# Kernel optimization log

Measured on AMD Instinct MI355X. Metric: run time of the kernel, lower is better.

The kernel has to match this reference:

```python
import jax, jax.numpy as jnp
import numpy as np

N = 4096
REG_STRENGTH = 1.0
BLOCK_EPS = 1e-6  # tolerance for detecting pooled-block boundaries in the backward


@jax.custom_vjp
def isotonic_l2(y):
    """argmin_{v_1 >= v_2 >= ... >= v_n} 0.5 * ||v - y||^2 (PAV solution).

    Computed via the exact minimax characterization, fully vectorized:
        v_i = min_{j <= i} max_{k >= i} mean(y[j..k])
    """
    return _iso_solution(y)


def _iso_solution(y):
    n = y.shape[0]
    cs = jnp.concatenate([jnp.zeros((1,), y.dtype), jnp.cumsum(y)])  # [n+1]
    idx = jnp.arange(n)
    j = idx[:, None]  # block start
    k = idx[None, :]  # block end
    length = (k - j + 1).astype(y.dtype)
    A = (cs[k + 1] - cs[j]) / length            # mean(y[j..k]) where k >= j
    A = jnp.where(k >= j, A, -jnp.inf)
    # M[j, i] = max_{k >= i} A[j, k]  (reverse cumulative max along k)
    M = jnp.flip(jax.lax.cummax(jnp.flip(A, axis=1), axis=1), axis=1)
    # v_i = min_{j <= i} M[j, i]  (cumulative min along j, take diagonal)
    v = jnp.diagonal(jax.lax.cummin(M, axis=0))
    return v


def _iso_fwd(y):
    v = _iso_solution(y)
    return v, v


def _iso_bwd(v, g):
    # Jacobian of PAV: within each pooled block, grad is the block mean of g.
    n = v.shape[0]
    drop = (v[:-1] - v[1:]) > BLOCK_EPS * jnp.maximum(jnp.abs(v[:-1]), 1.0)
    bid = jnp.concatenate([jnp.zeros((1,), jnp.int32),
                           jnp.cumsum(drop.astype(jnp.int32))])
    sums = jax.ops.segment_sum(g, bid, num_segments=n)
    cnts = jax.ops.segment_sum(jnp.ones_like(g), bid, num_segments=n)
    return ((sums / jnp.maximum(cnts, 1.0))[bid],)


isotonic_l2.defvjp(_iso_fwd, _iso_bwd)


def soft_rank(x, regularization_strength):
    """torchsort-style L2 soft rank: project x/eps onto permutahedron P([n..1])."""
    n = x.shape[0]
    theta = x / regularization_strength
    perm = jnp.argsort(-theta)          # descending sort permutation (constant wrt grad)
    s = theta[perm]
    w = jnp.arange(n, 0, -1, dtype=x.dtype)  # [n, n-1, ..., 1]
    sol = isotonic_l2(s - w)
    ranks_sorted = s - sol
    inv = jnp.argsort(perm)
    return ranks_sorted[inv]


def setup_inputs() -> dict:
    key = jax.random.key(0)
    kp, kt = jax.random.split(key)
    pred = jax.random.normal(kp, (N,), dtype=jnp.float32)
    target = jax.random.normal(kt, (N,), dtype=jnp.float32)
    return {"pred": pred, "target": target}


def reference(pred, target):
    p = soft_rank(pred, REG_STRENGTH)
    t = soft_rank(target, REG_STRENGTH)
    p = p - p.mean()
    p = p / jnp.linalg.norm(p)
    t = t - t.mean()
    t = t / jnp.linalg.norm(t)
    return 1.0 - jnp.sum(p * t)
```

## Files before the change

kernel.cpp:

```cpp
#include <hip/hip_runtime.h>
#include <math.h>

#define NEL   4096
#define NT    1024
#define HALF  512
#define EPT   (NEL / HALF)
#define CB    256

__global__ __launch_bounds__(CB)
void count_kernel(const float* __restrict__ pred,
                  const float* __restrict__ target,
                  int* __restrict__ counts) {
  __shared__ float jv[CB];
  const int arr = blockIdx.z;
  const float* __restrict__ x = arr ? target : pred;
  const int i     = blockIdx.x * CB + threadIdx.x;
  const int jbase = blockIdx.y * CB;

  jv[threadIdx.x] = x[jbase + threadIdx.x];
  const float xi = x[i];
  __syncthreads();

  int c = 0;
#pragma unroll 8
  for (int t = 0; t < CB; t++) {
    const float v = jv[t];
    const int   j = jbase + t;
    c += (v > xi || (v == xi && j < i)) ? 1 : 0;
  }
  atomicAdd(&counts[arr * NEL + i], c);
}

__global__ __launch_bounds__(NT)
void pav_loss_kernel(const float* __restrict__ pred,
                     const float* __restrict__ target,
                     const int* __restrict__ counts,
                     float* __restrict__ loss_out) {
  __shared__ float  s_val[2][NEL];
  __shared__ double s_P[2][NEL + 1];
  __shared__ int    s_cnt[2][NEL];
  __shared__ double s_wsum[2][HALF / 64];
  __shared__ int    s_nb[2];
  __shared__ double s_red[NT / 64][5];

  const int tid  = threadIdx.x;
  const int arr  = tid >> 9;
  const int tA   = tid & (HALF - 1);
  const int lane = tid & 63;
  const int wA   = tA >> 6;
  const float* __restrict__ x = arr ? target : pred;
  const int* __restrict__ cnt = counts + arr * NEL;
  const int base = tA * EPT;

  int   r[EPT];
  float xv[EPT];
#pragma unroll
  for (int e = 0; e < EPT; e++) {
    const int i = base + e;
    xv[e] = x[i];
    r[e]  = cnt[i];
    s_val[arr][r[e]] = xv[e];
  }
  __syncthreads();

  double c[EPT];
  double acc = 0.0;
#pragma unroll
  for (int e = 0; e < EPT; e++) {
    const int p = base + e;
    acc += (double)s_val[arr][p] - (double)(NEL - p);
    c[e] = acc;
  }
  double sc = acc;
#pragma unroll
  for (int d = 1; d < 64; d <<= 1) {
    const double o = __shfl_up(sc, d, 64);
    if (lane >= d) sc += o;
  }
  if (lane == 63) s_wsum[arr][wA] = sc;
  __syncthreads();
  if (tA == 0) {
    double a2 = 0.0;
    for (int w = 0; w < HALF / 64; w++) {
      const double t = s_wsum[arr][w];
      s_wsum[arr][w] = a2;
      a2 += t;
    }
  }
  __syncthreads();
  const double excl = s_wsum[arr][wA] + (sc - acc);
#pragma unroll
  for (int e = 0; e < EPT; e++) s_P[arr][base + e + 1] = excl + c[e];
  if (tA == 0) s_P[arr][0] = 0.0;
#pragma unroll
  for (int e = 0; e < EPT; e++) s_cnt[arr][base + e] = 1;
  __syncthreads();

  for (int m = 1; m < NEL; m <<= 1) {
    const int nmerge = NEL / (2 * m);
    for (int t = tA; t < nmerge; t += HALF) {
      const int lo = t * 2 * m, mid = lo + m, hi = lo + 2 * m;
      const int llen = s_cnt[arr][mid - 1];
      int cs = mid - llen;
      const int rlen = s_cnt[arr][mid];
      int ce = mid + rlen - 1;
      const double mL = (s_P[arr][mid] - s_P[arr][cs]) / (double)llen;
      const double mR = (s_P[arr][ce + 1] - s_P[arr][mid]) / (double)rlen;
      if (mL <= mR) {
        double mu = (s_P[arr][ce + 1] - s_P[arr][cs]) / (double)(ce - cs + 1);
        bool changed = true;
        while (changed) {
          changed = false;
          while (cs > lo) {
            const int l2 = s_cnt[arr][cs - 1];
            const double m2 = (s_P[arr][cs] - s_P[arr][cs - l2]) / (double)l2;
            if (m2 <= mu) {
              cs -= l2;
              mu = (s_P[arr][ce + 1] - s_P[arr][cs]) / (double)(ce - cs + 1);
              changed = true;
            } else break;
          }
          while (ce < hi - 1) {
            const int l2 = s_cnt[arr][ce + 1];
            const double m2 = (s_P[arr][ce + 1 + l2] - s_P[arr][ce + 1]) / (double)l2;
            if (m2 >= mu) {
              ce += l2;
              mu = (s_P[arr][ce + 1] - s_P[arr][cs]) / (double)(ce - cs + 1);
              changed = true;
            } else break;
          }
        }
        const int len = ce - cs + 1;
        s_cnt[arr][cs] = len;
        s_cnt[arr][ce] = len;
      }
    }
    __syncthreads();
  }

  if (tA == 0) {
    int s = 0, b = 0;
    while (s < NEL) {
      const int cc = s_cnt[arr][s];
      s_cnt[arr][b] = s;
      b++;
      s += cc;
    }
    s_nb[arr] = b;
  }
  __syncthreads();
  const int nb = s_nb[arr];

  float rv[EPT];
#pragma unroll
  for (int e = 0; e < EPT; e++) {
    const int p = base + e;
    int loB = 0, hiB = nb - 1;
    while (loB < hiB) {
      const int md = (loB + hiB + 1) >> 1;
      if (s_cnt[arr][md] <= p) loB = md; else hiB = md - 1;
    }
    const int st = s_cnt[arr][loB];
    const int en = (loB + 1 < nb) ? s_cnt[arr][loB + 1] : NEL;
    const double v = (s_P[arr][en] - s_P[arr][st]) / (double)(en - st);
    rv[e] = (float)((double)s_val[arr][p] - v);
  }
  __syncthreads();

  float* rs = (float*)s_cnt[arr];
#pragma unroll
  for (int e = 0; e < EPT; e++) rs[base + e] = rv[e];
  __syncthreads();

#pragma unroll
  for (int e = 0; e < EPT; e++) s_val[arr][base + e] = rs[r[e]];
  __syncthreads();

  double Sp = 0.0, St = 0.0, Spp = 0.0, Stt = 0.0, Spt = 0.0;
#pragma unroll
  for (int e = 0; e < NEL / NT; e++) {
    const int i = tid * (NEL / NT) + e;
    const double p = (double)s_val[0][i];
    const double t = (double)s_val[1][i];
    Sp += p; St += t; Spp += p * p; Stt += t * t; Spt += p * t;
  }
#pragma unroll
  for (int d = 32; d > 0; d >>= 1) {
    Sp  += __shfl_down(Sp,  d, 64);
    St  += __shfl_down(St,  d, 64);
    Spp += __shfl_down(Spp, d, 64);
    Stt += __shfl_down(Stt, d, 64);
    Spt += __shfl_down(Spt, d, 64);
  }
  const int wid = tid >> 6;
  if (lane == 0) {
    s_red[wid][0] = Sp;  s_red[wid][1] = St;  s_red[wid][2] = Spp;
    s_red[wid][3] = Stt; s_red[wid][4] = Spt;
  }
  __syncthreads();
  if (tid == 0) {
    double a0 = 0, a1 = 0, a2 = 0, a3 = 0, a4 = 0;
    for (int w = 0; w < NT / 64; w++) {
      a0 += s_red[w][0]; a1 += s_red[w][1]; a2 += s_red[w][2];
      a3 += s_red[w][3]; a4 += s_red[w][4];
    }
    const double n  = (double)NEL;
    const double mp = a0 / n, mt = a1 / n;
    const double cov = a4 - n * mp * mt;
    const double vp  = a2 - n * mp * mp;
    const double vt  = a3 - n * mt * mt;
    loss_out[0] = (float)(1.0 - cov / sqrt(vp * vt));
  }
}

extern "C" void kernel_launch(void* const* d_in, const int* in_sizes, int n_in,
                              void* d_out, int out_size, void* d_ws, size_t ws_size,
                              hipStream_t stream) {
  const float* pred   = (const float*)d_in[0];
  const float* target = (const float*)d_in[1];
  int*   counts = (int*)d_ws;
  float* out    = (float*)d_out;

  hipMemsetAsync(counts, 0, 2 * NEL * sizeof(int), stream);
  hipLaunchKernelGGL(count_kernel, dim3(NEL / CB, NEL / CB, 2), dim3(CB), 0,
                     stream, pred, target, counts);
  hipLaunchKernelGGL(pav_loss_kernel, dim3(1), dim3(NT), 0, stream,
                     pred, target, counts, out);
}
```

Measured before the change: 87.56 us.

## Drop memset and atomics, merge small PAV levels per thread, skip unsort pass

The rank-count kernel now writes per-segment partial counts over 4 larger j-segments with float4 shared reads, replacing the memset and atomicAdd. The PAV kernel sums those partials itself. Its thread count is halved so each thread owns 16 elements and runs the first merge levels locally without block barriers. The final scatter back to original order is replaced by gathering with stored ranks during the reduction. This cuts the number of kernel launches and __syncthreads, but leaves fewer threads for the later merge levels.

```diff
diff --git a/kernel.cpp b/kernel.cpp
--- a/kernel.cpp
+++ b/kernel.cpp
@@ -2,39 +2,46 @@
 #include <math.h>
 
 #define NEL   4096
-#define NT    1024
-#define HALF  512
+#define NT    512
+#define HALF  256
 #define EPT   (NEL / HALF)
+#define CPT   (NEL / NT)
+#define JSEG  4
+#define JLEN  (NEL / JSEG)
 #define CB    256
 
 __global__ __launch_bounds__(CB)
 void count_kernel(const float* __restrict__ pred,
                   const float* __restrict__ target,
-                  int* __restrict__ counts) {
-  __shared__ float jv[CB];
+                  int* __restrict__ part) {
+  __shared__ float jv[JLEN];
   const int arr = blockIdx.z;
   const float* __restrict__ x = arr ? target : pred;
   const int i     = blockIdx.x * CB + threadIdx.x;
-  const int jbase = blockIdx.y * CB;
-
-  jv[threadIdx.x] = x[jbase + threadIdx.x];
+  const int jbase = blockIdx.y * JLEN;
+
+  for (int t = threadIdx.x; t < JLEN; t += CB) jv[t] = x[jbase + t];
   const float xi = x[i];
   __syncthreads();
 
+  const float4* jv4 = (const float4*)jv;
   int c = 0;
-#pragma unroll 8
-  for (int t = 0; t < CB; t++) {
-    const float v = jv[t];
-    const int   j = jbase + t;
-    c += (v > xi || (v == xi && j < i)) ? 1 : 0;
-  }
-  atomicAdd(&counts[arr * NEL + i], c);
+#pragma unroll 4
+  for (int t4 = 0; t4 < JLEN / 4; t4++) {
+    const float4 v = jv4[t4];
+    const int j = jbase + t4 * 4;
+    c += (v.x > xi || (v.x == xi && j + 0 < i)) ? 1 : 0;
+    c += (v.y > xi || (v.y == xi && j + 1 < i)) ? 1 : 0;
+    c += (v.z > xi || (v.z == xi && j + 2 < i)) ? 1 : 0;
+    c += (v.w > xi || (v.w == xi && j + 3 < i)) ? 1 : 0;
+  }
+  part[(arr * JSEG + blockIdx.y) * NEL + i] = c;
 }
 
 __global__ __launch_bounds__(NT)
 void pav_loss_kernel(const float* __restrict__ pred,
                      const float* __restrict__ target,
-                     const int* __restrict__ counts,
+                     const int* __restrict__ part,
                      float* __restrict__ loss_out) {
   __shared__ float  s_val[2][NEL];
   __shared__ double s_P[2][NEL + 1];
@@ -44,12 +51,11 @@
   __shared__ double s_red[NT / 64][5];
 
   const int tid  = threadIdx.x;
-  const int arr  = tid >> 9;
+  const int arr  = tid >> 8;
   const int tA   = tid & (HALF - 1);
   const int lane = tid & 63;
   const int wA   = tA >> 6;
   const float* __restrict__ x = arr ? target : pred;
-  const int* __restrict__ cnt = counts + arr * NEL;
   const int base = tA * EPT;
 
   int   r[EPT];
@@ -57,10 +63,24 @@
 #pragma unroll
   for (int e = 0; e < EPT; e++) {
     const int i = base + e;
+    int c = 0;
+#pragma unroll
+    for (int s = 0; s < JSEG; s++) c += part[(arr * JSEG + s) * NEL + i];
+    r[e] = c;
+    s_cnt[arr][i] = c;
     xv[e] = x[i];
-    r[e]  = cnt[i];
-    s_val[arr][r[e]] = xv[e];
-  }
+  }
+  __syncthreads();
+
+  int rp[CPT], rt[CPT];
+#pragma unroll
+  for (int e = 0; e < CPT; e++) {
+    const int i = tid * CPT + e;
+    rp[e] = s_cnt[0][i];
+    rt[e] = s_cnt[1][i];
+  }
+#pragma unroll
+  for (int e = 0; e < EPT; e++) s_val[arr][r[e]] = xv[e];
   __syncthreads();
 
   double c[EPT];
@@ -96,7 +116,48 @@
   for (int e = 0; e < EPT; e++) s_cnt[arr][base + e] = 1;
   __syncthreads();
 
-  for (int m = 1; m < NEL; m <<= 1) {
+  for (int m = 1; m <= EPT / 2; m <<= 1) {
+    const int rpt = EPT / (2 * m);
+    for (int t = tA * rpt; t < (tA + 1) * rpt; t++) {
+      const int lo = t * 2 * m, mid = lo + m, hi = lo + 2 * m;
+      const int llen = s_cnt[arr][mid - 1];
+      int cs = mid - llen;
+      const int rlen = s_cnt[arr][mid];
+      int ce = mid + rlen - 1;
+      const double mL = (s_P[arr][mid] - s_P[arr][cs]) / (double)llen;
+      const double mR = (s_P[arr][ce + 1] - s_P[arr][mid]) / (double)rlen;
+      if (mL <= mR) {
+        double mu = (s_P[arr][ce + 1] - s_P[arr][cs]) / (double)(ce - cs + 1);
+        bool changed = true;
+        while (changed) {
+          changed = false;
+          while (cs > lo) {
+            const int l2 = s_cnt[arr][cs - 1];
+            const double m2 = (s_P[arr][cs] - s_P[arr][cs - l2]) / (double)l2;
+            if (m2 <= mu) {
+              cs -= l2;
+              mu = (s_P[arr][ce + 1] - s_P[arr][cs]) / (double)(ce - cs + 1);
+              changed = true;
+            } else break;
+          }
+          while (ce < hi - 1) {
+            const int l2 = s_cnt[arr][ce + 1];
+            const double m2 = (s_P[arr][ce + 1 + l2] - s_P[arr][ce + 1]) / (double)l2;
+            if (m2 >= mu) {
+              ce += l2;
+              mu = (s_P[arr][ce + 1] - s_P[arr][cs]) / (double)(ce - cs + 1);
+              changed = true;
+            } else break;
+          }
+        }
+        const int len = ce - cs + 1;
+        s_cnt[arr][cs] = len;
+        s_cnt[arr][ce] = len;
+      }
+    }
+  }
+  __syncthreads();
+  for (int m = EPT; m < NEL; m <<= 1) {
     const int nmerge = NEL / (2 * m);
     for (int t = tA; t < nmerge; t += HALF) {
       const int lo = t * 2 * m, mid = lo + m, hi = lo + 2 * m;
@@ -151,7 +212,6 @@
   __syncthreads();
   const int nb = s_nb[arr];
 
-  float rv[EPT];
 #pragma unroll
   for (int e = 0; e < EPT; e++) {
     const int p = base + e;
@@ -163,25 +223,15 @@
     const int st = s_cnt[arr][loB];
     const int en = (loB + 1 < nb) ? s_cnt[arr][loB + 1] : NEL;
     const double v = (s_P[arr][en] - s_P[arr][st]) / (double)(en - st);
-    rv[e] = (float)((double)s_val[arr][p] - v);
-  }
-  __syncthreads();
-
-  float* rs = (float*)s_cnt[arr];
-#pragma unroll
-  for (int e = 0; e < EPT; e++) rs[base + e] = rv[e];
-  __syncthreads();
-
-#pragma unroll
-  for (int e = 0; e < EPT; e++) s_val[arr][base + e] = rs[r[e]];
+    s_val[arr][p] = (float)((double)s_val[arr][p] - v);
+  }
   __syncthreads();
 
   double Sp = 0.0, St = 0.0, Spp = 0.0, Stt = 0.0, Spt = 0.0;
 #pragma unroll
-  for (int e = 0; e < NEL / NT; e++) {
-    const int i = tid * (NEL / NT) + e;
-    const double p = (double)s_val[0][i];
-    const double t = (double)s_val[1][i];
+  for (int e = 0; e < CPT; e++) {
+    const double p = (double)s_val[0][rp[e]];
+    const double t = (double)s_val[1][rt[e]];
     Sp += p; St += t; Spp += p * p; Stt += t * t; Spt += p * t;
   }
 #pragma unroll
@@ -218,12 +268,11 @@
                               hipStream_t stream) {
   const float* pred   = (const float*)d_in[0];
   const float* target = (const float*)d_in[1];
-  int*   counts = (int*)d_ws;
-  float* out    = (float*)d_out;
-
-  hipMemsetAsync(counts, 0, 2 * NEL * sizeof(int), stream);
-  hipLaunchKernelGGL(count_kernel, dim3(NEL / CB, NEL / CB, 2), dim3(CB), 0,
-                     stream, pred, target, counts);
+  int*   part = (int*)d_ws;
+  float* out  = (float*)d_out;
+
+  hipLaunchKernelGGL(count_kernel, dim3(NEL / CB, JSEG, 2), dim3(CB), 0,
+                     stream, pred, target, part);
   hipLaunchKernelGGL(pav_loss_kernel, dim3(1), dim3(NT), 0, stream,
-                     pred, target, counts, out);
+                     pred, target, part, out);
 }
```

After: 113.2 us. +29.3%, slower.
